# Kernel tuning notes

Hardware: AMD Instinct MI355X
Metric: run time of the kernel (lower is better)

## Reference

```python
import jax, jax.numpy as jnp
import numpy as np

BN_EPS = 1e-5

def binarize_ste(x):
    # sign() in forward; identity (straight-through) in backward, matching the
    # weight.data / input.data hack in BinarizeConv2d.
    return x + jax.lax.stop_gradient(jnp.sign(x) - x)


def setup_inputs() -> dict:
    key = jax.random.key(0)
    k1, k2, k3, k4 = jax.random.split(key, 4)
    N, Cin, H, W = 16, 32, 224, 224
    Cout, K = 32, 3
    x = jax.random.normal(k1, (N, Cin, H, W), dtype=jnp.float32)
    weight = jax.random.normal(k2, (Cout, Cin, K, K), dtype=jnp.float32) * 0.1
    gamma = jax.random.uniform(k3, (Cout,), dtype=jnp.float32, minval=0.5, maxval=1.5)
    beta = jax.random.normal(k4, (Cout,), dtype=jnp.float32) * 0.1
    return {"x": x, "weight": weight, "gamma": gamma, "beta": beta}


def reference(x, weight, gamma, beta):
    # BinarizeConv2d: binarize input iff C != 3, always binarize weights.
    xb = binarize_ste(x) if x.shape[1] != 3 else x
    wb = binarize_ste(weight)
    y = jax.lax.conv_general_dilated(
        xb, wb,
        window_strides=(1, 1),
        padding=((1, 1), (1, 1)),
        dimension_numbers=("NCHW", "OIHW", "NCHW"),
    )  # [N, Cout, H, W]
    # BatchNorm2d in training mode: per-channel batch statistics over (N, H, W).
    mean = jnp.mean(y, axis=(0, 2, 3))
    var = jnp.var(y, axis=(0, 2, 3))
    inv = jax.lax.rsqrt(var + BN_EPS)
    yn = (y - mean[None, :, None, None]) * inv[None, :, None, None]
    return yn * gamma[None, :, None, None] + beta[None, :, None, None]
```

## Files before the change

### kernel.cpp

```cpp
#include <hip/hip_runtime.h>
#include <stdint.h>

#define NB 16
#define CC 32
#define HH 224
#define WWID 224
#define HWS (HH*WWID)
#define NHWT (NB*HWS)
#define STRIPS (NHWT/4)
#define SPI (HWS/4)
#define SPR (WWID/4)

#define PITCH 232
#define PROWS 226
#define IMGW (PITCH*PROWS)

typedef float    f4 __attribute__((ext_vector_type(4)));
typedef unsigned u4 __attribute__((ext_vector_type(4)));
typedef unsigned u2 __attribute__((ext_vector_type(2)));

#define WS_WSIGN 0
#define WS_WNZ   2048
#define WS_BASE  4096
#define WS_FLAGW 5248
#define WS_FLAGZ 5252
#define WS_SSUM  5376
#define WS_SSQ   5632
#define WS_XS    8192
#define WS_XNZ   (8192 + (size_t)NB*IMGW*4)

__global__ void __launch_bounds__(256) pack_x4(
        const float* __restrict__ x, const float* __restrict__ w,
        unsigned* __restrict__ xs, unsigned* __restrict__ xnz,
        unsigned* __restrict__ wsg, unsigned* __restrict__ wnz,
        int* __restrict__ flagw, int* __restrict__ flagz, int* __restrict__ baset) {
    __shared__ unsigned s_sg[288];
    __shared__ int allnz;

    if (blockIdx.x == 0) {
        if (threadIdx.x == 0) allnz = 1;
        __syncthreads();
        for (int k = threadIdx.x; k < 288; k += 256) {
            int co = k / 9, tap = k % 9;
            unsigned bits = 0, nz = 0;
            for (int ci = 0; ci < CC; ++ci) {
                float v = w[(co * CC + ci) * 9 + tap];
                bits |= (v > 0.f ? 1u : 0u) << ci;
                nz   |= (v != 0.f ? 1u : 0u) << ci;
            }
            wsg[k] = bits; wnz[k] = nz; s_sg[k] = bits;
            if (nz != 0xffffffffu) atomicAnd(&allnz, 0);
        }
        __syncthreads();
        if (threadIdx.x == 0) *flagw = allnz;
        for (int k = threadIdx.x; k < 288; k += 256) {
            int cls = k >> 5, co = k & 31;
            int hc = cls / 3, wc = cls % 3;
            int nv = 0, corr = 0;
            #pragma unroll
            for (int kh = 0; kh < 3; ++kh)
                #pragma unroll
                for (int kw = 0; kw < 3; ++kw) {
                    bool inv = (hc == 0 && kh == 0) || (hc == 2 && kh == 2) ||
                               (wc == 0 && kw == 0) || (wc == 2 && kw == 2);
                    if (inv) corr += __popc(s_sg[co * 9 + kh * 3 + kw]);
                    else     nv++;
                }
            baset[k] = 32 * nv + 2 * corr;
        }
    }

    int t = blockIdx.x * 256 + threadIdx.x;
    int n = t / SPI, rem = t - n * SPI;
    int h = rem / SPR, w0 = (rem - h * SPR) * 4;
    const float* base = x + (size_t)n * CC * HWS + h * WWID + w0;
    unsigned b0=0,b1=0,b2=0,b3=0, z0=0,z1=0,z2=0,z3=0;
    #pragma unroll
    for (int c = 0; c < CC; ++c) {
        f4 v = __builtin_nontemporal_load((const f4*)(base + (size_t)c * HWS));
        b0 |= (v.x > 0.f ? (1u<<c) : 0u);  z0 |= (v.x != 0.f ? (1u<<c) : 0u);
        b1 |= (v.y > 0.f ? (1u<<c) : 0u);  z1 |= (v.y != 0.f ? (1u<<c) : 0u);
        b2 |= (v.z > 0.f ? (1u<<c) : 0u);  z2 |= (v.z != 0.f ? (1u<<c) : 0u);
        b3 |= (v.w > 0.f ? (1u<<c) : 0u);  z3 |= (v.w != 0.f ? (1u<<c) : 0u);
    }
    size_t rowb = (size_t)n * IMGW + (h + 1) * PITCH;
    size_t d = rowb + 1 + w0;
    xs[d+0]=b0; xs[d+1]=b1; xs[d+2]=b2; xs[d+3]=b3;
    xnz[d+0]=z0; xnz[d+1]=z1; xnz[d+2]=z2; xnz[d+3]=z3;

    if (w0 == 0)        { xs[rowb] = 0;       xnz[rowb] = 0; }
    if (w0 == WWID - 4) { xs[rowb + 225] = 0; xnz[rowb + 225] = 0; }
    if (h == 0) {
        size_t tr = (size_t)n * IMGW;
        #pragma unroll
        for (int j = 0; j < 4; ++j) { xs[tr + 1 + w0 + j] = 0; xnz[tr + 1 + w0 + j] = 0; }
        if (w0 == 0)        { xs[tr] = 0;       xnz[tr] = 0; }
        if (w0 == WWID - 4) { xs[tr + 225] = 0; xnz[tr + 225] = 0; }
    }
    if (h == HH - 1) {
        size_t br = (size_t)n * IMGW + (size_t)(PROWS - 1) * PITCH;
        #pragma unroll
        for (int j = 0; j < 4; ++j) { xs[br + 1 + w0 + j] = 0; xnz[br + 1 + w0 + j] = 0; }
        if (w0 == 0)        { xs[br] = 0;       xnz[br] = 0; }
        if (w0 == WWID - 4) { xs[br + 225] = 0; xnz[br + 225] = 0; }
    }

    bool hasz = (z0 & z1 & z2 & z3) != 0xffffffffu;
    if (__any(hasz) && (threadIdx.x & 63) == 0) atomicOr(flagz, 1);
}

__device__ __forceinline__ void loadwin(const unsigned* __restrict__ p, unsigned a[6]) {
    u4 lo = *(const u4*)p;
    u2 hi = *(const u2*)(p + 4);
    a[0]=lo.x; a[1]=lo.y; a[2]=lo.z; a[3]=lo.w; a[4]=hi.x; a[5]=hi.y;
}

__device__ __forceinline__ void ad4(const unsigned a0[6], const unsigned a1[6],
                                    const unsigned a2[6],
                                    const unsigned* __restrict__ q, int ad[4]) {
    unsigned q0=q[0],q1=q[1],q2=q[2],q3=q[3],q4=q[4],q5=q[5],q6=q[6],q7=q[7],q8=q[8];
    #pragma unroll
    for (int px = 0; px < 4; ++px) {
        ad[px] = __popc(a0[px]^q0) + __popc(a0[px+1]^q1) + __popc(a0[px+2]^q2)
               + __popc(a1[px]^q3) + __popc(a1[px+1]^q4) + __popc(a1[px+2]^q5)
               + __popc(a2[px]^q6) + __popc(a2[px+1]^q7) + __popc(a2[px+2]^q8);
    }
}

__device__ __forceinline__ void y4_slowc(const unsigned a0[6], const unsigned a1[6],
                                         const unsigned a2[6], const unsigned z0[6],
                                         const unsigned z1[6], const unsigned z2[6],
                                         const unsigned* __restrict__ qs,
                                         const unsigned* __restrict__ qz, int y[4]) {
    #pragma unroll
    for (int px = 0; px < 4; ++px) {
        int am = 0, ad = 0;
        #pragma unroll
        for (int kw = 0; kw < 3; ++kw) {
            unsigned m0 = z0[px+kw] & qz[kw];
            unsigned m1 = z1[px+kw] & qz[3+kw];
            unsigned m2 = z2[px+kw] & qz[6+kw];
            am += __popc(m0) + __popc(m1) + __popc(m2);
            ad += __popc((a0[px+kw]^qs[kw])   & m0)
                + __popc((a1[px+kw]^qs[3+kw]) & m1)
                + __popc((a2[px+kw]^qs[6+kw]) & m2);
        }
        y[px] = am - 2 * ad;
    }
}

__global__ void __launch_bounds__(256, 8) convstats(
        const unsigned* __restrict__ xs, const unsigned* __restrict__ xnz,
        const unsigned* __restrict__ wsg, const unsigned* __restrict__ wnz,
        const int* __restrict__ baset, const int* __restrict__ flagw,
        const int* __restrict__ flagz, int* __restrict__ s_sum,
        unsigned long long* __restrict__ s_sq) {
    __shared__ int sb[288];
    __shared__ int ls[4][8], lq[4][8];
    for (int i = threadIdx.x; i < 288; i += 256) sb[i] = baset[i];
    __syncthreads();

    int cobase = (blockIdx.x & 3) * 8;
    int sid = (blockIdx.x >> 2) * 256 + threadIdx.x;
    int n = sid / SPI, rem = sid - n * SPI;
    int h = rem / SPR, w0 = (rem - h * SPR) * 4;
    size_t off = (size_t)n * IMGW + h * PITCH + w0;

    unsigned a0[6], a1[6], a2[6];
    loadwin(xs + off, a0); loadwin(xs + off + PITCH, a1); loadwin(xs + off + 2*PITCH, a2);

    int sacc[8], qacc[8];
    bool fast = (*flagw != 0) && (*flagz == 0);
    if (fast) {
        int hc = (h == 0) ? 0 : ((h == HH-1) ? 6 : 3);
        int c0 = (hc + ((w0 == 0) ? 0 : 1)) * 32;
        int c1 = (hc + 1) * 32;
        int c3 = (hc + ((w0 == WWID-4) ? 2 : 1)) * 32;
        #pragma unroll
        for (int u = 0; u < 8; ++u) {
            int co = cobase + u;
            int ad[4];
            ad4(a0, a1, a2, wsg + co * 9, ad);
            int y0 = sb[c0 + co] - 2 * ad[0];
            int y1 = sb[c1 + co] - 2 * ad[1];
            int y2 = sb[c1 + co] - 2 * ad[2];
            int y3 = sb[c3 + co] - 2 * ad[3];
            sacc[u] = y0 + y1 + y2 + y3;
            qacc[u] = y0*y0 + y1*y1 + y2*y2 + y3*y3;
        }
    } else {
        unsigned z0[6], z1[6], z2[6];
        loadwin(xnz + off, z0); loadwin(xnz + off + PITCH, z1); loadwin(xnz + off + 2*PITCH, z2);
        #pragma unroll
        for (int u = 0; u < 8; ++u) {
            int co = cobase + u;
            int y[4];
            y4_slowc(a0, a1, a2, z0, z1, z2, wsg + co * 9, wnz + co * 9, y);
            sacc[u] = y[0]+y[1]+y[2]+y[3];
            qacc[u] = y[0]*y[0]+y[1]*y[1]+y[2]*y[2]+y[3]*y[3];
        }
    }

    #pragma unroll
    for (int o2 = 32; o2; o2 >>= 1) {
        #pragma unroll
        for (int u = 0; u < 8; ++u) {
            sacc[u] += __shfl_down(sacc[u], o2);
            qacc[u] += __shfl_down(qacc[u], o2);
        }
    }
    int wid = threadIdx.x >> 6, lane = threadIdx.x & 63;
    if (lane == 0) {
        #pragma unroll
        for (int u = 0; u < 8; ++u) { ls[wid][u] = sacc[u]; lq[wid][u] = qacc[u]; }
    }
    __syncthreads();
    if (threadIdx.x < 8) {
        int u = threadIdx.x;
        int S = ls[0][u] + ls[1][u] + ls[2][u] + ls[3][u];
        long long Q = (long long)lq[0][u] + lq[1][u] + lq[2][u] + lq[3][u];
        atomicAdd(&s_sum[cobase + u], S);
        atomicAdd(&s_sq[cobase + u], (unsigned long long)Q);
    }
}

__global__ void __launch_bounds__(256, 8) convnorm(
        const unsigned* __restrict__ xs, const unsigned* __restrict__ xnz,
        const unsigned* __restrict__ wsg, const unsigned* __restrict__ wnz,
        const int* __restrict__ baset, const int* __restrict__ flagw,
        const int* __restrict__ flagz, const int* __restrict__ s_sum,
        const unsigned long long* __restrict__ s_sq,
        const float* __restrict__ gamma, const float* __restrict__ beta,
        float* __restrict__ out) {
    __shared__ int sb[288];
    __shared__ float s_sc[32], s_sh[32];
    for (int i = threadIdx.x; i < 288; i += 256) sb[i] = baset[i];
    if (threadIdx.x < 32) {
        int c = threadIdx.x;
        double mean = (double)s_sum[c] / (double)NHWT;
        double var  = (double)(long long)s_sq[c] / (double)NHWT - mean * mean;
        float inv = (float)(1.0 / sqrt(var + 1e-5));
        float g = gamma[c] * inv;
        s_sc[c] = g;
        s_sh[c] = beta[c] - (float)mean * g;
    }
    __syncthreads();

    int cobase = (blockIdx.x & 3) * 8;
    int sid = (blockIdx.x >> 2) * 256 + threadIdx.x;
    int n = sid / SPI, rem = sid - n * SPI;
    int h = rem / SPR, w0 = (rem - h * SPR) * 4;
    size_t off = (size_t)n * IMGW + h * PITCH + w0;

    unsigned a0[6], a1[6], a2[6];
    loadwin(xs + off, a0); loadwin(xs + off + PITCH, a1); loadwin(xs + off + 2*PITCH, a2);

    float* on = out + (size_t)(n * CC + cobase) * HWS + h * WWID + w0;
    bool fast = (*flagw != 0) && (*flagz == 0);
    if (fast) {
        int hc = (h == 0) ? 0 : ((h == HH-1) ? 6 : 3);
        int c0 = (hc + ((w0 == 0) ? 0 : 1)) * 32;
        int c1 = (hc + 1) * 32;
        int c3 = (hc + ((w0 == WWID-4) ? 2 : 1)) * 32;
        #pragma unroll
        for (int u = 0; u < 8; ++u) {
            int co = cobase + u;
            int ad[4];
            ad4(a0, a1, a2, wsg + co * 9, ad);
            int y0 = sb[c0 + co] - 2 * ad[0];
            int y1 = sb[c1 + co] - 2 * ad[1];
            int y2 = sb[c1 + co] - 2 * ad[2];
            int y3 = sb[c3 + co] - 2 * ad[3];
            float sc = s_sc[co], sh = s_sh[co];
            f4 o = { fmaf((float)y0, sc, sh), fmaf((float)y1, sc, sh),
                     fmaf((float)y2, sc, sh), fmaf((float)y3, sc, sh) };
            *(f4*)(on + (size_t)u * HWS) = o;
        }
    } else {
        unsigned z0[6], z1[6], z2[6];
        loadwin(xnz + off, z0); loadwin(xnz + off + PITCH, z1); loadwin(xnz + off + 2*PITCH, z2);
        #pragma unroll
        for (int u = 0; u < 8; ++u) {
            int co = cobase + u;
            int y[4];
            y4_slowc(a0, a1, a2, z0, z1, z2, wsg + co * 9, wnz + co * 9, y);
            float sc = s_sc[co], sh = s_sh[co];
            f4 o = { fmaf((float)y[0], sc, sh), fmaf((float)y[1], sc, sh),
                     fmaf((float)y[2], sc, sh), fmaf((float)y[3], sc, sh) };
            *(f4*)(on + (size_t)u * HWS) = o;
        }
    }
}

extern "C" void kernel_launch(void* const* d_in, const int* in_sizes, int n_in,
                              void* d_out, int out_size, void* d_ws, size_t ws_size,
                              hipStream_t stream) {
    const float* x     = (const float*)d_in[0];
    const float* w     = (const float*)d_in[1];
    const float* gamma = (const float*)d_in[2];
    const float* beta  = (const float*)d_in[3];
    float* out = (float*)d_out;

    char* ws = (char*)d_ws;
    unsigned* wsg            = (unsigned*)(ws + WS_WSIGN);
    unsigned* wnz            = (unsigned*)(ws + WS_WNZ);
    int* baset               = (int*)(ws + WS_BASE);
    int* flagw               = (int*)(ws + WS_FLAGW);
    int* flagz               = (int*)(ws + WS_FLAGZ);
    int* s_sum               = (int*)(ws + WS_SSUM);
    unsigned long long* s_sq = (unsigned long long*)(ws + WS_SSQ);
    unsigned* xsb            = (unsigned*)(ws + WS_XS);
    unsigned* xzb            = (unsigned*)(ws + WS_XNZ);

    hipMemsetAsync(ws + WS_FLAGW, 0, 640, stream);

    int cgrid = STRIPS / 256 * 4;
    pack_x4  <<<STRIPS / 256, 256, 0, stream>>>(x, w, xsb, xzb, wsg, wnz,
                                                flagw, flagz, baset);
    convstats<<<cgrid, 256, 0, stream>>>(xsb, xzb, wsg, wnz, baset, flagw, flagz,
                                         s_sum, s_sq);
    convnorm <<<cgrid, 256, 0, stream>>>(xsb, xzb, wsg, wnz, baset, flagw, flagz,
                                         s_sum, s_sq, gamma, beta, out);
}
```

Baseline: 81.23 us.

## Replace global zero-flag atomic and memset with per-block flags and parallel reduction

```diff
diff --git a/kernel.cpp b/kernel.cpp
--- a/kernel.cpp
+++ b/kernel.cpp
@@ -10,6 +10,7 @@
 #define STRIPS (NHWT/4)
 #define SPI (HWS/4)
 #define SPR (WWID/4)
+#define PBLK (STRIPS/256)
 
 #define PITCH 232
 #define PROWS 226
@@ -23,22 +24,26 @@
 #define WS_WNZ   2048
 #define WS_BASE  4096
 #define WS_FLAGW 5248
-#define WS_FLAGZ 5252
 #define WS_SSUM  5376
 #define WS_SSQ   5632
-#define WS_XS    8192
-#define WS_XNZ   (8192 + (size_t)NB*IMGW*4)
+#define WS_BLKF  6144
+#define WS_XS    12288
+#define WS_XNZ   (12288 + (size_t)NB*IMGW*4)
 
 __global__ void __launch_bounds__(256) pack_x4(
         const float* __restrict__ x, const float* __restrict__ w,
         unsigned* __restrict__ xs, unsigned* __restrict__ xnz,
         unsigned* __restrict__ wsg, unsigned* __restrict__ wnz,
-        int* __restrict__ flagw, int* __restrict__ flagz, int* __restrict__ baset) {
+        int* __restrict__ flagw, unsigned* __restrict__ blkflag,
+        int* __restrict__ baset, int* __restrict__ s_sum,
+        unsigned long long* __restrict__ s_sq) {
     __shared__ unsigned s_sg[288];
     __shared__ int allnz;
+    __shared__ unsigned s_zf[4];
 
     if (blockIdx.x == 0) {
         if (threadIdx.x == 0) allnz = 1;
+        if (threadIdx.x < CC) { s_sum[threadIdx.x] = 0; s_sq[threadIdx.x] = 0ull; }
         __syncthreads();
         for (int k = threadIdx.x; k < 288; k += 256) {
             int co = k / 9, tap = k % 9;
@@ -106,7 +111,12 @@
     }
 
     bool hasz = (z0 & z1 & z2 & z3) != 0xffffffffu;
-    if (__any(hasz) && (threadIdx.x & 63) == 0) atomicOr(flagz, 1);
+    bool anyz = __any(hasz);
+    int wid = threadIdx.x >> 6, lane = threadIdx.x & 63;
+    if (lane == 0) s_zf[wid] = anyz ? 1u : 0u;
+    __syncthreads();
+    if (threadIdx.x == 0)
+        blkflag[blockIdx.x] = s_zf[0] | s_zf[1] | s_zf[2] | s_zf[3];
 }
 
 __device__ __forceinline__ void loadwin(const unsigned* __restrict__ p, unsigned a[6]) {
@@ -149,16 +159,21 @@
     }
 }
 
+__device__ __forceinline__ unsigned zf_load(const unsigned* __restrict__ blkflag, int t) {
+    unsigned zv = blkflag[t] | blkflag[t + 256] | blkflag[t + 512];
+    if (t < PBLK - 768) zv |= blkflag[t + 768];
+    return zv;
+}
+
 __global__ void __launch_bounds__(256, 8) convstats(
         const unsigned* __restrict__ xs, const unsigned* __restrict__ xnz,
         const unsigned* __restrict__ wsg, const unsigned* __restrict__ wnz,
         const int* __restrict__ baset, const int* __restrict__ flagw,
-        const int* __restrict__ flagz, int* __restrict__ s_sum,
+        const unsigned* __restrict__ blkflag, int* __restrict__ s_sum,
         unsigned long long* __restrict__ s_sq) {
     __shared__ int sb[288];
-    __shared__ int ls[4][8], lq[4][8];
-    for (int i = threadIdx.x; i < 288; i += 256) sb[i] = baset[i];
-    __syncthreads();
+    __shared__ unsigned s_zf[4];
+    __shared__ int red[4][8][17];
 
     int cobase = (blockIdx.x & 3) * 8;
     int sid = (blockIdx.x >> 2) * 256 + threadIdx.x;
@@ -169,8 +184,16 @@
     unsigned a0[6], a1[6], a2[6];
     loadwin(xs + off, a0); loadwin(xs + off + PITCH, a1); loadwin(xs + off + 2*PITCH, a2);
 
+    int t = threadIdx.x, wid = t >> 6, lane = t & 63;
+    unsigned zv = zf_load(blkflag, t);
+    int fw = *flagw;
+    for (int i = t; i < 288; i += 256) sb[i] = baset[i];
+    bool anyz = __any(zv != 0);
+    if (lane == 0) s_zf[wid] = anyz ? 1u : 0u;
+    __syncthreads();
+    bool fast = (fw != 0) && ((s_zf[0] | s_zf[1] | s_zf[2] | s_zf[3]) == 0u);
+
     int sacc[8], qacc[8];
-    bool fast = (*flagw != 0) && (*flagz == 0);
     if (fast) {
         int hc = (h == 0) ? 0 : ((h == HH-1) ? 6 : 3);
         int c0 = (hc + ((w0 == 0) ? 0 : 1)) * 32;
@@ -202,25 +225,30 @@
     }
 
     #pragma unroll
-    for (int o2 = 32; o2; o2 >>= 1) {
+    for (int o2 = 32; o2 >= 8; o2 >>= 1) {
         #pragma unroll
         for (int u = 0; u < 8; ++u) {
             sacc[u] += __shfl_down(sacc[u], o2);
             qacc[u] += __shfl_down(qacc[u], o2);
         }
     }
-    int wid = threadIdx.x >> 6, lane = threadIdx.x & 63;
-    if (lane == 0) {
-        #pragma unroll
-        for (int u = 0; u < 8; ++u) { ls[wid][u] = sacc[u]; lq[wid][u] = qacc[u]; }
+    if (lane < 8) {
+        #pragma unroll
+        for (int u = 0; u < 8; ++u) {
+            red[wid][lane][u]     = sacc[u];
+            red[wid][lane][8 + u] = qacc[u];
+        }
     }
     __syncthreads();
-    if (threadIdx.x < 8) {
-        int u = threadIdx.x;
-        int S = ls[0][u] + ls[1][u] + ls[2][u] + ls[3][u];
-        long long Q = (long long)lq[0][u] + lq[1][u] + lq[2][u] + lq[3][u];
-        atomicAdd(&s_sum[cobase + u], S);
-        atomicAdd(&s_sq[cobase + u], (unsigned long long)Q);
+    if (t < 128) {
+        int u16 = t >> 3, s = t & 7;
+        int v = red[0][s][u16] + red[1][s][u16] + red[2][s][u16] + red[3][s][u16];
+        v += __shfl_down(v, 4); v += __shfl_down(v, 2); v += __shfl_down(v, 1);
+        if (s == 0) {
+            if (u16 < 8) atomicAdd(&s_sum[cobase + u16], v);
+            else         atomicAdd(&s_sq[cobase + u16 - 8],
+                                   (unsigned long long)(long long)v);
+        }
     }
 }
 
@@ -228,15 +256,29 @@
         const unsigned* __restrict__ xs, const unsigned* __restrict__ xnz,
         const unsigned* __restrict__ wsg, const unsigned* __restrict__ wnz,
         const int* __restrict__ baset, const int* __restrict__ flagw,
-        const int* __restrict__ flagz, const int* __restrict__ s_sum,
+        const unsigned* __restrict__ blkflag, const int* __restrict__ s_sum,
         const unsigned long long* __restrict__ s_sq,
         const float* __restrict__ gamma, const float* __restrict__ beta,
         float* __restrict__ out) {
     __shared__ int sb[288];
     __shared__ float s_sc[32], s_sh[32];
-    for (int i = threadIdx.x; i < 288; i += 256) sb[i] = baset[i];
-    if (threadIdx.x < 32) {
-        int c = threadIdx.x;
+    __shared__ unsigned s_zf[4];
+
+    int cobase = (blockIdx.x & 3) * 8;
+    int sid = (blockIdx.x >> 2) * 256 + threadIdx.x;
+    int n = sid / SPI, rem = sid - n * SPI;
+    int h = rem / SPR, w0 = (rem - h * SPR) * 4;
+    size_t off = (size_t)n * IMGW + h * PITCH + w0;
+
+    unsigned a0[6], a1[6], a2[6];
+    loadwin(xs + off, a0); loadwin(xs + off + PITCH, a1); loadwin(xs + off + 2*PITCH, a2);
+
+    int t = threadIdx.x, wid = t >> 6, lane = t & 63;
+    unsigned zv = zf_load(blkflag, t);
+    int fw = *flagw;
+    for (int i = t; i < 288; i += 256) sb[i] = baset[i];
+    if (t < 32) {
+        int c = t;
         double mean = (double)s_sum[c] / (double)NHWT;
         double var  = (double)(long long)s_sq[c] / (double)NHWT - mean * mean;
         float inv = (float)(1.0 / sqrt(var + 1e-5));
@@ -244,19 +286,12 @@
         s_sc[c] = g;
         s_sh[c] = beta[c] - (float)mean * g;
     }
+    bool anyz = __any(zv != 0);
+    if (lane == 0) s_zf[wid] = anyz ? 1u : 0u;
     __syncthreads();
-
-    int cobase = (blockIdx.x & 3) * 8;
-    int sid = (blockIdx.x >> 2) * 256 + threadIdx.x;
-    int n = sid / SPI, rem = sid - n * SPI;
-    int h = rem / SPR, w0 = (rem - h * SPR) * 4;
-    size_t off = (size_t)n * IMGW + h * PITCH + w0;
-
-    unsigned a0[6], a1[6], a2[6];
-    loadwin(xs + off, a0); loadwin(xs + off + PITCH, a1); loadwin(xs + off + 2*PITCH, a2);
+    bool fast = (fw != 0) && ((s_zf[0] | s_zf[1] | s_zf[2] | s_zf[3]) == 0u);
 
     float* on = out + (size_t)(n * CC + cobase) * HWS + h * WWID + w0;
-    bool fast = (*flagw != 0) && (*flagz == 0);
     if (fast) {
         int hc = (h == 0) ? 0 : ((h == HH-1) ? 6 : 3);
         int c0 = (hc + ((w0 == 0) ? 0 : 1)) * 32;
@@ -306,19 +341,17 @@
     unsigned* wnz            = (unsigned*)(ws + WS_WNZ);
     int* baset               = (int*)(ws + WS_BASE);
     int* flagw               = (int*)(ws + WS_FLAGW);
-    int* flagz               = (int*)(ws + WS_FLAGZ);
     int* s_sum               = (int*)(ws + WS_SSUM);
     unsigned long long* s_sq = (unsigned long long*)(ws + WS_SSQ);
+    unsigned* blkflag        = (unsigned*)(ws + WS_BLKF);
     unsigned* xsb            = (unsigned*)(ws + WS_XS);
     unsigned* xzb            = (unsigned*)(ws + WS_XNZ);
 
-    hipMemsetAsync(ws + WS_FLAGW, 0, 640, stream);
-
-    int cgrid = STRIPS / 256 * 4;
-    pack_x4  <<<STRIPS / 256, 256, 0, stream>>>(x, w, xsb, xzb, wsg, wnz,
-                                                flagw, flagz, baset);
-    convstats<<<cgrid, 256, 0, stream>>>(xsb, xzb, wsg, wnz, baset, flagw, flagz,
+    int cgrid = PBLK * 4;
+    pack_x4  <<<PBLK, 256, 0, stream>>>(x, w, xsb, xzb, wsg, wnz,
+                                        flagw, blkflag, baset, s_sum, s_sq);
+    convstats<<<cgrid, 256, 0, stream>>>(xsb, xzb, wsg, wnz, baset, flagw, blkflag,
                                          s_sum, s_sq);
-    convnorm <<<cgrid, 256, 0, stream>>>(xsb, xzb, wsg, wnz, baset, flagw, flagz,
+    convnorm <<<cgrid, 256, 0, stream>>>(xsb, xzb, wsg, wnz, baset, flagw, blkflag,
                                          s_sum, s_sq, gamma, beta, out);
 }
```

Result: faster. 77.93 us (median of 2 runs) (-4.1%).
